# Optimization experiments

Measured on AMD Instinct MI355X. Metric: run time of the kernel, lower is better.

Reference implementation:

```python
import jax, jax.numpy as jnp
import numpy as np

BS, NS, NM, NO = 262144, 16, 8, 8

def setup_inputs() -> dict:
    key = jax.random.key(0)
    k = jax.random.split(key, 6)
    z = jax.random.normal(k[0], (BS, NM), dtype=jnp.float32)
    x0 = jax.random.normal(k[1], (BS, NS), dtype=jnp.float32)
    A = jax.random.normal(k[2], (BS, NS, NS), dtype=jnp.float32) * 0.1
    # PSD initial covariance per batch element
    P0 = jnp.einsum('bij,bkj->bik', A, A) + jnp.eye(NS, dtype=jnp.float32)
    phi = jnp.eye(NS, dtype=jnp.float32) + 0.01 * jax.random.normal(k[3], (NS, NS), dtype=jnp.float32)
    H = jax.random.normal(k[4], (NM, NS), dtype=jnp.float32) * 0.3
    C = jax.random.normal(k[5], (NO, NS), dtype=jnp.float32) * 0.3
    Qdiag = jnp.full((NS,), 0.1, dtype=jnp.float32)
    Rdiag = jnp.full((NM,), 0.1, dtype=jnp.float32)
    return {"z": z, "x0": x0, "P0": P0, "phi": phi, "H": H, "C": C,
            "Qdiag": Qdiag, "Rdiag": Rdiag}

def reference(z, x0, P0, phi, H, C, Qdiag, Rdiag):
    # --- predict ---
    x_pred = x0 @ phi.T                                       # [bs, ns]
    P_pred = jnp.einsum('ij,bjk,lk->bil', phi, P0, phi) + jnp.diag(Qdiag)  # phi P phi^T + Q
    # --- innovation ---
    y = z - x_pred @ H.T                                      # [bs, nm]
    S = jnp.einsum('ij,bjk,lk->bil', H, P_pred, H) + jnp.diag(Rdiag)       # H P H^T + R
    Sinv = jnp.linalg.inv(S)                                  # [bs, nm, nm]
    # --- gain and update ---
    K = jnp.einsum('bij,kj,bkl->bil', P_pred, H, Sinv)        # P H^T S^-1 [bs, ns, nm]
    x_new = x_pred + jnp.einsum('bij,bj->bi', K, y)           # [bs, ns]
    P_new = P_pred - jnp.einsum('bij,jk,bkl->bil', K, H, P_pred)  # (I - K H) P
    out = x_new @ C.T                                         # [bs, no]
    return out
```

## Files before the change

### kernel.cpp

```cpp
#include <hip/hip_runtime.h>


#define QFMA(ACC, OFF, A, V) { ACC[(OFF)+0] += (A)*(V).x; ACC[(OFF)+1] += (A)*(V).y; ACC[(OFF)+2] += (A)*(V).z; ACC[(OFF)+3] += (A)*(V).w; }
#define TS 132
#define XS 28
#define TRI(a,k) ((a)*((a)+1)/2 + (k))

__global__ __launch_bounds__(256) void kalman_fused9(
    const float* __restrict__ z,
    const float* __restrict__ x0,
    const float* __restrict__ P0,
    const float* __restrict__ phi,
    const float* __restrict__ Hm,
    const float* __restrict__ Cm,
    const float* __restrict__ Qd,
    const float* __restrict__ Rd,
    float* __restrict__ out,
    int bs)
{
    __shared__ __align__(16) float BnS[8 * 20];
    __shared__ __align__(16) float BTS[16 * 8];
    __shared__ __align__(16) float CpS[8 * 20];
    __shared__ __align__(16) float CQHS[8 * 8];
    __shared__ __align__(16) float ScS[8 * 8];
    __shared__ __align__(16) float x0S[32 * XS];
    __shared__ __align__(16) float Tb[32 * TS];

    const int tid = threadIdx.x;
    const int e = tid >> 3;
    const int i = tid & 7;
    long b = (long)blockIdx.x * 32 + e;
    const bool valid = (b < (long)bs);
    if (!valid) b = (long)bs - 1;

    float4 Pq[8];
    {
        const float4* P0v = reinterpret_cast<const float4*>(P0 + (size_t)b * 256);
#pragma unroll
        for (int q = 0; q < 4; ++q) {
            Pq[q]     = P0v[i * 4 + q];
            Pq[q + 4] = P0v[(i + 8) * 4 + q];
        }
    }
    const float x0a = x0[b * 16 + i];
    const float x0b = x0[b * 16 + 8 + i];
    float yv = z[b * 8 + i];
    x0S[e * XS + i]     = x0a;
    x0S[e * XS + i + 8] = x0b;

    if (tid < 128) {
        const int m = tid >> 4, k = tid & 15;
        float bv = 0.f, cv = 0.f;
#pragma unroll
        for (int j = 0; j < 16; ++j) {
            const float pj = phi[j * 16 + k];
            bv += Hm[m * 16 + j] * pj;
            cv += Cm[m * 16 + j] * pj;
        }
        BnS[m * 20 + k] = bv;
        BTS[k * 8 + m]  = bv;
        CpS[m * 20 + k] = cv;
    }
    if (tid < 64) {
        const int i2 = tid >> 3, j2 = tid & 7;
        float sc = (i2 == j2) ? Rd[i2] : 0.f;
        float cq = 0.f;
#pragma unroll
        for (int k = 0; k < 16; ++k) {
            const float qh = Qd[k] * Hm[j2 * 16 + k];
            sc += Hm[i2 * 16 + k] * qh;
            cq += Cm[i2 * 16 + k] * qh;
        }
        ScS[i2 * 8 + j2]  = sc;
        CQHS[i2 * 8 + j2] = cq;
    }
    __syncthreads();

    float t0[8], t1[8];
#pragma unroll
    for (int m = 0; m < 8; ++m) { t0[m] = 0.f; t1[m] = 0.f; }
#pragma unroll
    for (int q = 0; q < 4; ++q) {
        const float4 A = Pq[q], B4 = Pq[q + 4];
        const float a[4] = {A.x, A.y, A.z, A.w};
        const float c[4] = {B4.x, B4.y, B4.z, B4.w};
#pragma unroll
        for (int kk = 0; kk < 4; ++kk) {
            const int k = 4 * q + kk;
            const float4 b0v = *reinterpret_cast<const float4*>(&BTS[k * 8 + 0]);
            const float4 b1v = *reinterpret_cast<const float4*>(&BTS[k * 8 + 4]);
            QFMA(t0, 0, a[kk], b0v) QFMA(t0, 4, a[kk], b1v)
            QFMA(t1, 0, c[kk], b0v) QFMA(t1, 4, c[kk], b1v)
        }
    }
    *reinterpret_cast<float4*>(&Tb[e * TS + i * 8 + 0]) = make_float4(t0[0], t0[1], t0[2], t0[3]);
    *reinterpret_cast<float4*>(&Tb[e * TS + i * 8 + 4]) = make_float4(t0[4], t0[5], t0[6], t0[7]);
    *reinterpret_cast<float4*>(&Tb[e * TS + (i + 8) * 8 + 0]) = make_float4(t1[0], t1[1], t1[2], t1[3]);
    *reinterpret_cast<float4*>(&Tb[e * TS + (i + 8) * 8 + 4]) = make_float4(t1[4], t1[5], t1[6], t1[7]);

    float br[16];
#pragma unroll
    for (int q = 0; q < 4; ++q) {
        const float4 A = *reinterpret_cast<const float4*>(&BnS[i * 20 + 4 * q]);
        br[4*q+0] = A.x; br[4*q+1] = A.y; br[4*q+2] = A.z; br[4*q+3] = A.w;
    }

    float s[8];
    {
        const float4 c0 = *reinterpret_cast<const float4*>(&ScS[i * 8 + 0]);
        const float4 c1 = *reinterpret_cast<const float4*>(&ScS[i * 8 + 4]);
        s[0]=c0.x; s[1]=c0.y; s[2]=c0.z; s[3]=c0.w; s[4]=c1.x; s[5]=c1.y; s[6]=c1.z; s[7]=c1.w;
    }
#pragma unroll
    for (int j = 0; j < 16; ++j) {
        const float4 ta = *reinterpret_cast<const float4*>(&Tb[e * TS + j * 8 + 0]);
        const float4 tb = *reinterpret_cast<const float4*>(&Tb[e * TS + j * 8 + 4]);
        const float bij = br[j];
        QFMA(s, 0, bij, ta) QFMA(s, 4, bij, tb)
    }

#pragma unroll
    for (int q = 0; q < 4; ++q) {
        const float4 X = *reinterpret_cast<const float4*>(&x0S[e * XS + 4 * q]);
        yv -= br[4*q+0]*X.x + br[4*q+1]*X.y + br[4*q+2]*X.z + br[4*q+3]*X.w;
    }

    *reinterpret_cast<float4*>(&Tb[e * TS + i * 8 + 0]) = make_float4(s[0], s[1], s[2], s[3]);
    *reinterpret_cast<float4*>(&Tb[e * TS + i * 8 + 4]) = make_float4(s[4], s[5], s[6], s[7]);
    x0S[e * XS + 16 + i] = yv;

    float L[36];
#pragma unroll
    for (int a = 0; a < 8; ++a) {
        const float4 q0 = *reinterpret_cast<const float4*>(&Tb[e * TS + a * 8 + 0]);
        L[TRI(a,0)] = q0.x;
        if (a >= 1) L[TRI(a,1)] = q0.y;
        if (a >= 2) L[TRI(a,2)] = q0.z;
        if (a >= 3) L[TRI(a,3)] = q0.w;
        if (a >= 4) {
            const float4 q1 = *reinterpret_cast<const float4*>(&Tb[e * TS + a * 8 + 4]);
            L[TRI(a,4)] = q1.x;
            if (a >= 5) L[TRI(a,5)] = q1.y;
            if (a >= 6) L[TRI(a,6)] = q1.z;
            if (a >= 7) L[TRI(a,7)] = q1.w;
        }
    }
    float yf[8];
    {
        const float4 ya = *reinterpret_cast<const float4*>(&x0S[e * XS + 16]);
        const float4 yb = *reinterpret_cast<const float4*>(&x0S[e * XS + 20]);
        yf[0]=ya.x; yf[1]=ya.y; yf[2]=ya.z; yf[3]=ya.w;
        yf[4]=yb.x; yf[5]=yb.y; yf[6]=yb.z; yf[7]=yb.w;
    }

#pragma unroll
    for (int k = 0; k < 8; ++k) {
        const float inv = __builtin_amdgcn_rsqf(L[TRI(k,k)]);
        L[TRI(k,k)] = inv;
#pragma unroll
        for (int a = k + 1; a < 8; ++a) L[TRI(a,k)] *= inv;
#pragma unroll
        for (int a = k + 1; a < 8; ++a) {
#pragma unroll
            for (int m = k + 1; m <= a; ++m)
                L[TRI(a,m)] -= L[TRI(a,k)] * L[TRI(m,k)];
        }
    }
#pragma unroll
    for (int a = 0; a < 8; ++a) {
        float t = yf[a];
#pragma unroll
        for (int j = 0; j < a; ++j) t -= L[TRI(a,j)] * yf[j];
        yf[a] = t * L[TRI(a,a)];
    }
#pragma unroll
    for (int a = 7; a >= 0; --a) {
        float t = yf[a];
#pragma unroll
        for (int j = a + 1; j < 8; ++j) t -= L[TRI(j,a)] * yf[j];
        yf[a] = t * L[TRI(a,a)];
    }

    float th0 = 0.f, th1 = 0.f;
#pragma unroll
    for (int m = 0; m < 8; ++m) { th0 += t0[m] * yf[m]; th1 += t1[m] * yf[m]; }
    x0S[e * XS + i]     = x0a + th0;
    x0S[e * XS + i + 8] = x0b + th1;

    float oc = 0.f;
#pragma unroll
    for (int q = 0; q < 4; ++q) {
        const float4 A = *reinterpret_cast<const float4*>(&CpS[i * 20 + 4 * q]);
        const float4 U = *reinterpret_cast<const float4*>(&x0S[e * XS + 4 * q]);
        oc += A.x*U.x + A.y*U.y + A.z*U.z + A.w*U.w;
    }
    {
        const float4 q0 = *reinterpret_cast<const float4*>(&CQHS[i * 8 + 0]);
        const float4 q1 = *reinterpret_cast<const float4*>(&CQHS[i * 8 + 4]);
        oc += q0.x*yf[0] + q0.y*yf[1] + q0.z*yf[2] + q0.w*yf[3]
            + q1.x*yf[4] + q1.y*yf[5] + q1.z*yf[6] + q1.w*yf[7];
    }
    if (valid) out[b * 8 + i] = oc;
}

extern "C" void kernel_launch(void* const* d_in, const int* in_sizes, int n_in,
                              void* d_out, int out_size, void* d_ws, size_t ws_size,
                              hipStream_t stream)
{
    const float* z   = (const float*)d_in[0];
    const float* x0  = (const float*)d_in[1];
    const float* P0  = (const float*)d_in[2];
    const float* phi = (const float*)d_in[3];
    const float* H   = (const float*)d_in[4];
    const float* C   = (const float*)d_in[5];
    const float* Qd  = (const float*)d_in[6];
    const float* Rd  = (const float*)d_in[7];
    float* out = (float*)d_out;

    const int bs = in_sizes[0] / 8;
    const int blocks = (bs + 31) / 32;
    hipLaunchKernelGGL(kalman_fused9, dim3(blocks), dim3(256), 0, stream,
                       z, x0, P0, phi, H, C, Qd, Rd, out, bs);
}
```

Measured before the change: 69.48 us.

## Precompute derived constant matrices once in a separate kernel, read from global

The per-block computation of H·phi, C·phi, HQH^T+R and CQH^T moves into a single-block prep kernel that writes them to workspace. The main kernel then reads these constants straight from global memory (cached, uniform across threads) instead of recomputing them into shared memory. This removes the redundant per-block prologue and its __syncthreads, at the cost of a second kernel launch and global/scalar loads in the inner loops.

```diff
diff --git a/kernel.cpp b/kernel.cpp
--- a/kernel.cpp
+++ b/kernel.cpp
@@ -1,28 +1,56 @@
 #include <hip/hip_runtime.h>
 
 
-#define QFMA(ACC, OFF, A, V) { ACC[(OFF)+0] += (A)*(V).x; ACC[(OFF)+1] += (A)*(V).y; ACC[(OFF)+2] += (A)*(V).z; ACC[(OFF)+3] += (A)*(V).w; }
 #define TS 132
 #define XS 28
 #define TRI(a,k) ((a)*((a)+1)/2 + (k))
 
-__global__ __launch_bounds__(256) void kalman_fused9(
-    const float* __restrict__ z,
-    const float* __restrict__ x0,
-    const float* __restrict__ P0,
+
+__global__ __launch_bounds__(128) void kalman_derive(
     const float* __restrict__ phi,
     const float* __restrict__ Hm,
     const float* __restrict__ Cm,
     const float* __restrict__ Qd,
     const float* __restrict__ Rd,
+    float* __restrict__ cst)
+{
+    const int tid = threadIdx.x;
+    {
+        const int m = tid >> 4, k = tid & 15;
+        float bv = 0.f, cv = 0.f;
+#pragma unroll
+        for (int j = 0; j < 16; ++j) {
+            const float pj = phi[j * 16 + k];
+            bv += Hm[m * 16 + j] * pj;
+            cv += Cm[m * 16 + j] * pj;
+        }
+        cst[m * 16 + k]        = bv;
+        cst[128 + m * 16 + k]  = cv;
+        cst[384 + k * 8 + m]   = bv;
+    }
+    if (tid < 64) {
+        const int i2 = tid >> 3, j2 = tid & 7;
+        float sc = (i2 == j2) ? Rd[i2] : 0.f;
+        float cq = 0.f;
+#pragma unroll
+        for (int k = 0; k < 16; ++k) {
+            const float qh = Qd[k] * Hm[j2 * 16 + k];
+            sc += Hm[i2 * 16 + k] * qh;
+            cq += Cm[i2 * 16 + k] * qh;
+        }
+        cst[256 + i2 * 8 + j2] = sc;
+        cst[320 + i2 * 8 + j2] = cq;
+    }
+}
+
+__global__ __launch_bounds__(256) void kalman_fused11(
+    const float* __restrict__ z,
+    const float* __restrict__ x0,
+    const float* __restrict__ P0,
+    const float* __restrict__ cst,
     float* __restrict__ out,
     int bs)
 {
-    __shared__ __align__(16) float BnS[8 * 20];
-    __shared__ __align__(16) float BTS[16 * 8];
-    __shared__ __align__(16) float CpS[8 * 20];
-    __shared__ __align__(16) float CQHS[8 * 8];
-    __shared__ __align__(16) float ScS[8 * 8];
     __shared__ __align__(16) float x0S[32 * XS];
     __shared__ __align__(16) float Tb[32 * TS];
 
@@ -48,34 +76,14 @@
     x0S[e * XS + i]     = x0a;
     x0S[e * XS + i + 8] = x0b;
 
-    if (tid < 128) {
-        const int m = tid >> 4, k = tid & 15;
-        float bv = 0.f, cv = 0.f;
-#pragma unroll
-        for (int j = 0; j < 16; ++j) {
-            const float pj = phi[j * 16 + k];
-            bv += Hm[m * 16 + j] * pj;
-            cv += Cm[m * 16 + j] * pj;
-        }
-        BnS[m * 20 + k] = bv;
-        BTS[k * 8 + m]  = bv;
-        CpS[m * 20 + k] = cv;
-    }
-    if (tid < 64) {
-        const int i2 = tid >> 3, j2 = tid & 7;
-        float sc = (i2 == j2) ? Rd[i2] : 0.f;
-        float cq = 0.f;
-#pragma unroll
-        for (int k = 0; k < 16; ++k) {
-            const float qh = Qd[k] * Hm[j2 * 16 + k];
-            sc += Hm[i2 * 16 + k] * qh;
-            cq += Cm[i2 * 16 + k] * qh;
-        }
-        ScS[i2 * 8 + j2]  = sc;
-        CQHS[i2 * 8 + j2] = cq;
-    }
-    __syncthreads();
-
+    float br[16];
+#pragma unroll
+    for (int q = 0; q < 4; ++q) {
+        const float4 A = *reinterpret_cast<const float4*>(&cst[i * 16 + 4 * q]);
+        br[4*q+0] = A.x; br[4*q+1] = A.y; br[4*q+2] = A.z; br[4*q+3] = A.w;
+    }
+
+    const float* __restrict__ BT = cst + 384;
     float t0[8], t1[8];
 #pragma unroll
     for (int m = 0; m < 8; ++m) { t0[m] = 0.f; t1[m] = 0.f; }
@@ -87,10 +95,12 @@
 #pragma unroll
         for (int kk = 0; kk < 4; ++kk) {
             const int k = 4 * q + kk;
-            const float4 b0v = *reinterpret_cast<const float4*>(&BTS[k * 8 + 0]);
-            const float4 b1v = *reinterpret_cast<const float4*>(&BTS[k * 8 + 4]);
-            QFMA(t0, 0, a[kk], b0v) QFMA(t0, 4, a[kk], b1v)
-            QFMA(t1, 0, c[kk], b0v) QFMA(t1, 4, c[kk], b1v)
+#pragma unroll
+            for (int m = 0; m < 8; ++m) {
+                const float Bkm = BT[k * 8 + m];
+                t0[m] += a[kk] * Bkm;
+                t1[m] += c[kk] * Bkm;
+            }
         }
     }
     *reinterpret_cast<float4*>(&Tb[e * TS + i * 8 + 0]) = make_float4(t0[0], t0[1], t0[2], t0[3]);
@@ -98,17 +108,10 @@
     *reinterpret_cast<float4*>(&Tb[e * TS + (i + 8) * 8 + 0]) = make_float4(t1[0], t1[1], t1[2], t1[3]);
     *reinterpret_cast<float4*>(&Tb[e * TS + (i + 8) * 8 + 4]) = make_float4(t1[4], t1[5], t1[6], t1[7]);
 
-    float br[16];
-#pragma unroll
-    for (int q = 0; q < 4; ++q) {
-        const float4 A = *reinterpret_cast<const float4*>(&BnS[i * 20 + 4 * q]);
-        br[4*q+0] = A.x; br[4*q+1] = A.y; br[4*q+2] = A.z; br[4*q+3] = A.w;
-    }
-
     float s[8];
     {
-        const float4 c0 = *reinterpret_cast<const float4*>(&ScS[i * 8 + 0]);
-        const float4 c1 = *reinterpret_cast<const float4*>(&ScS[i * 8 + 4]);
+        const float4 c0 = *reinterpret_cast<const float4*>(&cst[256 + i * 8 + 0]);
+        const float4 c1 = *reinterpret_cast<const float4*>(&cst[256 + i * 8 + 4]);
         s[0]=c0.x; s[1]=c0.y; s[2]=c0.z; s[3]=c0.w; s[4]=c1.x; s[5]=c1.y; s[6]=c1.z; s[7]=c1.w;
     }
 #pragma unroll
@@ -116,7 +119,8 @@
         const float4 ta = *reinterpret_cast<const float4*>(&Tb[e * TS + j * 8 + 0]);
         const float4 tb = *reinterpret_cast<const float4*>(&Tb[e * TS + j * 8 + 4]);
         const float bij = br[j];
-        QFMA(s, 0, bij, ta) QFMA(s, 4, bij, tb)
+        s[0] += bij*ta.x; s[1] += bij*ta.y; s[2] += bij*ta.z; s[3] += bij*ta.w;
+        s[4] += bij*tb.x; s[5] += bij*tb.y; s[6] += bij*tb.z; s[7] += bij*tb.w;
     }
 
 #pragma unroll
@@ -190,13 +194,13 @@
     float oc = 0.f;
 #pragma unroll
     for (int q = 0; q < 4; ++q) {
-        const float4 A = *reinterpret_cast<const float4*>(&CpS[i * 20 + 4 * q]);
+        const float4 A = *reinterpret_cast<const float4*>(&cst[128 + i * 16 + 4 * q]);
         const float4 U = *reinterpret_cast<const float4*>(&x0S[e * XS + 4 * q]);
         oc += A.x*U.x + A.y*U.y + A.z*U.z + A.w*U.w;
     }
     {
-        const float4 q0 = *reinterpret_cast<const float4*>(&CQHS[i * 8 + 0]);
-        const float4 q1 = *reinterpret_cast<const float4*>(&CQHS[i * 8 + 4]);
+        const float4 q0 = *reinterpret_cast<const float4*>(&cst[320 + i * 8 + 0]);
+        const float4 q1 = *reinterpret_cast<const float4*>(&cst[320 + i * 8 + 4]);
         oc += q0.x*yf[0] + q0.y*yf[1] + q0.z*yf[2] + q0.w*yf[3]
             + q1.x*yf[4] + q1.y*yf[5] + q1.z*yf[6] + q1.w*yf[7];
     }
@@ -216,9 +220,13 @@
     const float* Qd  = (const float*)d_in[6];
     const float* Rd  = (const float*)d_in[7];
     float* out = (float*)d_out;
+    float* cst = (float*)d_ws;
 
     const int bs = in_sizes[0] / 8;
     const int blocks = (bs + 31) / 32;
-    hipLaunchKernelGGL(kalman_fused9, dim3(blocks), dim3(256), 0, stream,
-                       z, x0, P0, phi, H, C, Qd, Rd, out, bs);
+
+    hipLaunchKernelGGL(kalman_derive, dim3(1), dim3(128), 0, stream,
+                       phi, H, C, Qd, Rd, cst);
+    hipLaunchKernelGGL(kalman_fused11, dim3(blocks), dim3(256), 0, stream,
+                       z, x0, P0, cst, out, bs);
 }
```

After: 75.97 us. 9.3% more time.
